# Optimization experiments

Measured on AMD Instinct MI355X. Metric: run time of the kernel, lower is better.

## Reference

```python
import jax, jax.numpy as jnp
import numpy as np

EPS = 1e-8  # torch.cosine_similarity eps


def setup_inputs() -> dict:
    key = jax.random.key(0)
    kq, km, ki = jax.random.split(key, 3)
    B, N, D = 512, 131072, 512
    query = jax.random.normal(kq, (B, D), dtype=jnp.float32)
    memory_matrix = jax.random.normal(km, (N, D), dtype=jnp.float32)
    importance = jax.random.uniform(ki, (N,), dtype=jnp.float32)
    return {"query": query, "memory_matrix": memory_matrix, "importance": importance, "k": 16}


def reference(query, memory_matrix, importance, k):
    # Cosine similarity (torch semantics: dot / max(|q||m|, eps))
    q_norm = jnp.linalg.norm(query, axis=-1)            # [B]
    m_norm = jnp.linalg.norm(memory_matrix, axis=-1)    # [N]
    dots = jnp.einsum('bd,nd->bn', query, memory_matrix)  # [B, N]
    sims = dots / jnp.maximum(q_norm[:, None] * m_norm[None, :], EPS)
    # Importance boosting
    boosted = sims * (1.0 + 0.3 * importance)[None, :]
    # Top-k retrieval + gather of memory contents
    vals, idx = jax.lax.top_k(boosted, k)               # [B, k]
    gathered = memory_matrix[idx]                        # [B, k, D]
    return vals, gathered
```

## Files before the change

kernel.cpp:

```cpp
#include <hip/hip_runtime.h>
#include <hip/hip_bf16.h>
#include <math.h>

#define BQ 512
#define DIM 512
#define NMEM 131072
#define TOPK 16

#define BM 128
#define BN 128
#define BK 32
#define KSTEPS (DIM / BK)
#define NSUB 8
#define CHUNK_N (BN * NSUB)
#define CHUNKS (NMEM / CHUNK_N)
#define BTILES (BQ / BM)
#define CAP 32
#define CAPF 24
#define RESCORE 32
#define LDSTR 40
#define NEG_INF (-3.402823466e38f)

typedef unsigned short u16;
typedef unsigned int u32;
typedef short bf16x8 __attribute__((ext_vector_type(8)));
typedef float f32x4 __attribute__((ext_vector_type(4)));

static __device__ inline u32 pack2(float a, float b) {
  __hip_bfloat162 p = __float22bfloat162_rn(make_float2(a, b));
  return *(u32*)&p;
}

static __device__ inline void gl_lds16(const void* g, void* l) {
  __builtin_amdgcn_global_load_lds(
      (const __attribute__((address_space(1))) u32*)g,
      (__attribute__((address_space(3))) u32*)l, 16, 0, 0);
}

__global__ __launch_bounds__(256) void prep_kernel(const float* __restrict__ q,
                                                   float* __restrict__ inv_qn,
                                                   u16* __restrict__ qb) {
  int row = blockIdx.x * 4 + (threadIdx.x >> 6);
  int lane = threadIdx.x & 63;
  const float4* r4 = (const float4*)(q + (size_t)row * DIM);
  float4 x0 = r4[lane * 2], x1 = r4[lane * 2 + 1];
  float ss = x0.x * x0.x + x0.y * x0.y + x0.z * x0.z + x0.w * x0.w +
             x1.x * x1.x + x1.y * x1.y + x1.z * x1.z + x1.w * x1.w;
#pragma unroll
  for (int off = 32; off; off >>= 1) ss += __shfl_down(ss, off);
  if (lane == 0) inv_qn[row] = 1.0f / sqrtf(ss);
  uint4 w;
  w.x = pack2(x0.x, x0.y);
  w.y = pack2(x0.z, x0.w);
  w.z = pack2(x1.x, x1.y);
  w.w = pack2(x1.z, x1.w);
  *(uint4*)(qb + (size_t)row * DIM + lane * 8) = w;
}

__global__ __launch_bounds__(256) void convert_kernel(
    const float* __restrict__ mem, const float* __restrict__ imp,
    u16* __restrict__ membf, float* __restrict__ colscale) {
  int row = blockIdx.x * 4 + (threadIdx.x >> 6);
  int lane = threadIdx.x & 63;
  const float4* r4 = (const float4*)(mem + (size_t)row * DIM);
  float4 x0 = r4[lane * 2], x1 = r4[lane * 2 + 1];
  float ss = x0.x * x0.x + x0.y * x0.y + x0.z * x0.z + x0.w * x0.w +
             x1.x * x1.x + x1.y * x1.y + x1.z * x1.z + x1.w * x1.w;
  uint4 w;
  w.x = pack2(x0.x, x0.y);
  w.y = pack2(x0.z, x0.w);
  w.z = pack2(x1.x, x1.y);
  w.w = pack2(x1.z, x1.w);
  *(uint4*)(membf + (size_t)row * DIM + lane * 8) = w;
#pragma unroll
  for (int off = 32; off; off >>= 1) ss += __shfl_down(ss, off);
  if (lane == 0) colscale[row] = (1.0f + 0.3f * imp[row]) / sqrtf(ss);
}

static __device__ inline void mfma_step(const u16* Asb, const u16* Bsb, int wm,
                                        int wn, int c16, int quad,
                                        f32x4 acc[4][4]) {
  bf16x8 af[4], bfr[4];
  const int ksw = (quad ^ (c16 & 3)) * 8;
#pragma unroll
  for (int mi = 0; mi < 4; ++mi)
    af[mi] = *(const bf16x8*)&Asb[(wm * 64 + mi * 16 + c16) * BK + ksw];
#pragma unroll
  for (int ni = 0; ni < 4; ++ni)
    bfr[ni] = *(const bf16x8*)&Bsb[(wn * 64 + ni * 16 + c16) * BK + ksw];
#pragma unroll
  for (int mi = 0; mi < 4; ++mi)
#pragma unroll
    for (int ni = 0; ni < 4; ++ni)
      acc[mi][ni] = __builtin_amdgcn_mfma_f32_16x16x32_bf16(af[mi], bfr[ni],
                                                            acc[mi][ni], 0, 0, 0);
}

static __device__ inline void stage4(const u16* ag0, const u16* ag1,
                                     const u16* bg0, const u16* bg1, u16* Asb,
                                     u16* Bsb, int blk0, int blk1, int koff) {
  gl_lds16(ag0 + koff, Asb + blk0 * 512);
  gl_lds16(ag1 + koff, Asb + blk1 * 512);
  gl_lds16(bg0 + koff, Bsb + blk0 * 512);
  gl_lds16(bg1 + koff, Bsb + blk1 * 512);
}

__global__ __launch_bounds__(256, 2) void main_fast(
    const u16* __restrict__ qb, const u16* __restrict__ membf,
    const float* __restrict__ cs, const float* __restrict__ inv_qn,
    float* __restrict__ part_v, int* __restrict__ part_i) {
  __shared__ __align__(16) u16 As[2][BM * BK];
  __shared__ __align__(16) u16 Bs[2][BN * BK];
  __shared__ float topv[BM][TOPK];
  __shared__ int topi[BM][TOPK];
  __shared__ float cbv[BM * CAPF];
  __shared__ int cbi[BM * CAPF];
  __shared__ float cutoff[BM];
  __shared__ int cnt[BM];
  __shared__ float qn_s[BM];
  __shared__ int again;

  const int tid = threadIdx.x;
  const int lane = tid & 63, wid = tid >> 6;
  const int wm = wid >> 1, wn = wid & 1;
  const int c16 = lane & 15, quad = lane >> 4;

  const int lin = blockIdx.x;
  const int btile = (lin >> 3) & 3;
  const int chunk = (lin & 7) + ((lin >> 5) << 3);
  const int bbase = btile * BM;

  for (int e = tid; e < BM * TOPK; e += 256) {
    topv[e >> 4][e & 15] = NEG_INF;
    topi[e >> 4][e & 15] = -1;
  }
  if (tid < BM) {
    cutoff[tid] = NEG_INF;
    cnt[tid] = 0;
    qn_s[tid] = inv_qn[bbase + tid];
  }
  if (tid == 0) again = 0;
  __syncthreads();

  float qnl[16];
#pragma unroll
  for (int ii = 0; ii < 16; ++ii)
    qnl[ii] = qn_s[wm * 64 + (ii >> 2) * 16 + quad * 4 + (ii & 3)];

  const int blk0 = wid * 2, blk1 = wid * 2 + 1;
  const int rin = lane >> 2;
  const int sr0 = blk0 * 16 + rin;
  const int sr1 = blk1 * 16 + rin;
  const int skof = (((lane & 3) ^ (rin & 3)) * 8);
  const u16* ag0 = qb + (size_t)(bbase + sr0) * DIM + skof;
  const u16* ag1 = qb + (size_t)(bbase + sr1) * DIM + skof;

  for (int sub = 0; sub < NSUB; ++sub) {
    const int n0g = chunk * CHUNK_N + sub * BN;
    const u16* bg0 = membf + (size_t)(n0g + sr0) * DIM + skof;
    const u16* bg1 = membf + (size_t)(n0g + sr1) * DIM + skof;

    f32x4 acc[4][4];
#pragma unroll
    for (int mi = 0; mi < 4; ++mi)
#pragma unroll
      for (int ni = 0; ni < 4; ++ni) acc[mi][ni] = (f32x4){0.f, 0.f, 0.f, 0.f};

    stage4(ag0, ag1, bg0, bg1, &As[0][0], &Bs[0][0], blk0, blk1, 0);
    __syncthreads();

    for (int kp = 0; kp < KSTEPS / 2; ++kp) {
      stage4(ag0, ag1, bg0, bg1, &As[1][0], &Bs[1][0], blk0, blk1,
             (2 * kp + 1) * BK);
      mfma_step(&As[0][0], &Bs[0][0], wm, wn, c16, quad, acc);
      __syncthreads();
      if (kp + 1 < KSTEPS / 2)
        stage4(ag0, ag1, bg0, bg1, &As[0][0], &Bs[0][0], blk0, blk1,
               (2 * kp + 2) * BK);
      mfma_step(&As[1][0], &Bs[1][0], wm, wn, c16, quad, acc);
      __syncthreads();
    }

    float scl[4];
    int gcol[4];
#pragma unroll
    for (int ni = 0; ni < 4; ++ni) {
      const int c = n0g + wn * 64 + ni * 16 + c16;
      scl[ni] = cs[c];
      gcol[ni] = c;
    }
#pragma unroll
    for (int mi = 0; mi < 4; ++mi)
#pragma unroll
      for (int ni = 0; ni < 4; ++ni)
#pragma unroll
        for (int reg = 0; reg < 4; ++reg)
          acc[mi][ni][reg] *= qnl[mi * 4 + reg] * scl[ni];

    unsigned long long consumed = 0ull;
    for (;;) {
      float cutl[16];
#pragma unroll
      for (int ii = 0; ii < 16; ++ii)
        cutl[ii] = cutoff[wm * 64 + (ii >> 2) * 16 + quad * 4 + (ii & 3)];
#pragma unroll
      for (int mi = 0; mi < 4; ++mi)
#pragma unroll
        for (int reg = 0; reg < 4; ++reg) {
          const int r = wm * 64 + mi * 16 + quad * 4 + reg;
          const float cl = cutl[mi * 4 + reg];
#pragma unroll
          for (int ni = 0; ni < 4; ++ni) {
            const int bit = mi * 16 + ni * 4 + reg;
            const float v = acc[mi][ni][reg];
            if (!((consumed >> bit) & 1ull) && v > cl) {
              int pos = atomicAdd(&cnt[r], 1);
              if (pos < CAPF) {
                cbv[r * CAPF + pos] = v;
                cbi[r * CAPF + pos] = gcol[ni];
                consumed |= 1ull << bit;
              }
            }
          }
        }
      __syncthreads();
      if (tid < BM) {
        const int r = tid;
        const int m = cnt[r];
        const int take = m < CAPF ? m : CAPF;
        for (int c = 0; c < take; ++c) {
          const float v = cbv[r * CAPF + c];
          const int id = cbi[r * CAPF + c];
          if (v > topv[r][TOPK - 1]) {
            int j = TOPK - 1;
            while (j > 0 && topv[r][j - 1] < v) {
              topv[r][j] = topv[r][j - 1];
              topi[r][j] = topi[r][j - 1];
              --j;
            }
            topv[r][j] = v;
            topi[r][j] = id;
          }
        }
        cutoff[r] = topv[r][TOPK - 1];
        if (m > CAPF) again = 1;
        cnt[r] = 0;
      }
      __syncthreads();
      const int more = again;
      __syncthreads();
      if (tid == 0) again = 0;
      if (!more) break;
    }
  }

  for (int e = tid; e < BM * TOPK; e += 256) {
    const int r = e >> 4, j = e & 15;
    const size_t o = ((size_t)(bbase + r) * CHUNKS + chunk) * TOPK + j;
    part_v[o] = topv[r][j];
    part_i[o] = topi[r][j];
  }
}

__global__ __launch_bounds__(256, 2) void main_kernel(
    const u16* __restrict__ qb, const float* __restrict__ mem,
    const float* __restrict__ imp, const float* __restrict__ inv_qn,
    float* __restrict__ part_v, int* __restrict__ part_i) {
  __shared__ __align__(16) u16 As[BM * LDSTR];
  __shared__ __align__(16) u16 Bs[BN * LDSTR];
  __shared__ float topv[BM][TOPK];
  __shared__ int topi[BM][TOPK];
  __shared__ float cbv[BM * CAP];
  __shared__ int cbi[BM * CAP];
  __shared__ float cutoff[BM];
  __shared__ int cnt[BM];
  __shared__ float qn_s[BM];
  __shared__ float msum[BM * 4];
  __shared__ float colscale[BN];
  __shared__ int again;

  const int tid = threadIdx.x;
  const int lane = tid & 63, wid = tid >> 6;
  const int wm = wid >> 1, wn = wid & 1;
  const int c16 = lane & 15, quad = lane >> 4;

  const int lin = blockIdx.x;
  const int btile = (lin >> 3) & 3;
  const int chunk = (lin & 7) + ((lin >> 5) << 3);
  const int bbase = btile * BM;

  for (int e = tid; e < BM * TOPK; e += 256) {
    topv[e >> 4][e & 15] = NEG_INF;
    topi[e >> 4][e & 15] = -1;
  }
  if (tid < BM) {
    cutoff[tid] = NEG_INF;
    cnt[tid] = 0;
    qn_s[tid] = inv_qn[bbase + tid];
  }
  if (tid == 0) again = 0;
  __syncthreads();

  float qnl[16];
#pragma unroll
  for (int ii = 0; ii < 16; ++ii)
    qnl[ii] = qn_s[wm * 64 + (ii >> 2) * 16 + quad * 4 + (ii & 3)];

  const int arow = tid >> 2, akc = tid & 3;
  const u16* qsrc0 = qb + (size_t)(bbase + arow) * DIM + akc * 8;
  const u16* qsrc1 = qsrc0 + (size_t)64 * DIM;
  u16* adst0 = As + arow * LDSTR + akc * 8;
  u16* adst1 = adst0 + 64 * LDSTR;
  u16* bdst0 = Bs + arow * LDSTR + akc * 8;
  u16* bdst1 = bdst0 + 64 * LDSTR;

  for (int sub = 0; sub < NSUB; ++sub) {
    const int n0g = chunk * CHUNK_N + sub * BN;
    const float* bsrc0 = mem + (size_t)(n0g + arow) * DIM + akc * 8;
    const float* bsrc1 = bsrc0 + (size_t)64 * DIM;

    f32x4 acc[4][4];
#pragma unroll
    for (int mi = 0; mi < 4; ++mi)
#pragma unroll
      for (int ni = 0; ni < 4; ++ni) acc[mi][ni] = (f32x4){0.f, 0.f, 0.f, 0.f};
    float ss0 = 0.f, ss1 = 0.f;

    for (int kt = 0; kt < DIM / BK; ++kt) {
      const int k0 = kt * BK;
      uint4 qa0 = *(const uint4*)(qsrc0 + k0);
      uint4 qa1 = *(const uint4*)(qsrc1 + k0);
      float4 b0a = *(const float4*)(bsrc0 + k0);
      float4 b0b = *(const float4*)(bsrc0 + k0 + 4);
      float4 b1a = *(const float4*)(bsrc1 + k0);
      float4 b1b = *(const float4*)(bsrc1 + k0 + 4);
      ss0 += b0a.x * b0a.x + b0a.y * b0a.y + b0a.z * b0a.z + b0a.w * b0a.w +
             b0b.x * b0b.x + b0b.y * b0b.y + b0b.z * b0b.z + b0b.w * b0b.w;
      ss1 += b1a.x * b1a.x + b1a.y * b1a.y + b1a.z * b1a.z + b1a.w * b1a.w +
             b1b.x * b1b.x + b1b.y * b1b.y + b1b.z * b1b.z + b1b.w * b1b.w;
      __syncthreads();
      *(uint4*)adst0 = qa0;
      *(uint4*)adst1 = qa1;
      uint4 w0, w1;
      w0.x = pack2(b0a.x, b0a.y); w0.y = pack2(b0a.z, b0a.w);
      w0.z = pack2(b0b.x, b0b.y); w0.w = pack2(b0b.z, b0b.w);
      w1.x = pack2(b1a.x, b1a.y); w1.y = pack2(b1a.z, b1a.w);
      w1.z = pack2(b1b.x, b1b.y); w1.w = pack2(b1b.z, b1b.w);
      *(uint4*)bdst0 = w0;
      *(uint4*)bdst1 = w1;
      __syncthreads();
      bf16x8 af[4], bfr[4];
#pragma unroll
      for (int mi = 0; mi < 4; ++mi)
        af[mi] = *(const bf16x8*)&As[(wm * 64 + mi * 16 + c16) * LDSTR + quad * 8];
#pragma unroll
      for (int ni = 0; ni < 4; ++ni)
        bfr[ni] = *(const bf16x8*)&Bs[(wn * 64 + ni * 16 + c16) * LDSTR + quad * 8];
#pragma unroll
      for (int mi = 0; mi < 4; ++mi)
#pragma unroll
        for (int ni = 0; ni < 4; ++ni)
          acc[mi][ni] = __builtin_amdgcn_mfma_f32_16x16x32_bf16(
              af[mi], bfr[ni], acc[mi][ni], 0, 0, 0);
    }

    msum[arow * 4 + akc] = ss0;
    msum[(arow + 64) * 4 + akc] = ss1;
    __syncthreads();
    if (tid < BN)
      colscale[tid] = (1.0f + 0.3f * imp[n0g + tid]) /
                      sqrtf(msum[tid * 4] + msum[tid * 4 + 1] +
                            msum[tid * 4 + 2] + msum[tid * 4 + 3]);
    __syncthreads();

    float scl[4];
    int gcol[4];
#pragma unroll
    for (int ni = 0; ni < 4; ++ni) {
      scl[ni] = colscale[wn * 64 + ni * 16 + c16];
      gcol[ni] = n0g + wn * 64 + ni * 16 + c16;
    }
#pragma unroll
    for (int mi = 0; mi < 4; ++mi)
#pragma unroll
      for (int ni = 0; ni < 4; ++ni)
#pragma unroll
        for (int reg = 0; reg < 4; ++reg)
          acc[mi][ni][reg] *= qnl[mi * 4 + reg] * scl[ni];

    unsigned long long consumed = 0ull;
    for (;;) {
      float cutl[16];
#pragma unroll
      for (int ii = 0; ii < 16; ++ii)
        cutl[ii] = cutoff[wm * 64 + (ii >> 2) * 16 + quad * 4 + (ii & 3)];
#pragma unroll
      for (int mi = 0; mi < 4; ++mi)
#pragma unroll
        for (int reg = 0; reg < 4; ++reg) {
          const int r = wm * 64 + mi * 16 + quad * 4 + reg;
          const float cl = cutl[mi * 4 + reg];
#pragma unroll
          for (int ni = 0; ni < 4; ++ni) {
            const int bit = mi * 16 + ni * 4 + reg;
            const float v = acc[mi][ni][reg];
            if (!((consumed >> bit) & 1ull) && v > cl) {
              int pos = atomicAdd(&cnt[r], 1);
              if (pos < CAP) {
                cbv[r * CAP + pos] = v;
                cbi[r * CAP + pos] = gcol[ni];
                consumed |= 1ull << bit;
              }
            }
          }
        }
      __syncthreads();
      if (tid < BM) {
        const int r = tid;
        const int m = cnt[r];
        const int take = m < CAP ? m : CAP;
        for (int c = 0; c < take; ++c) {
          const float v = cbv[r * CAP + c];
          const int id = cbi[r * CAP + c];
          if (v > topv[r][TOPK - 1]) {
            int j = TOPK - 1;
            while (j > 0 && topv[r][j - 1] < v) {
              topv[r][j] = topv[r][j - 1];
              topi[r][j] = topi[r][j - 1];
              --j;
            }
            topv[r][j] = v;
            topi[r][j] = id;
          }
        }
        cutoff[r] = topv[r][TOPK - 1];
        if (m > CAP) again = 1;
        cnt[r] = 0;
      }
      __syncthreads();
      const int more = again;
      __syncthreads();
      if (tid == 0) again = 0;
      if (!more) break;
    }
  }

  for (int e = tid; e < BM * TOPK; e += 256) {
    const int r = e >> 4, j = e & 15;
    const size_t o = ((size_t)(bbase + r) * CHUNKS + chunk) * TOPK + j;
    part_v[o] = topv[r][j];
    part_i[o] = topi[r][j];
  }
}

#define CAND (CHUNKS * TOPK)
__global__ __launch_bounds__(256) void final_kernel(
    const float* __restrict__ part_v, const int* __restrict__ part_i,
    const float* __restrict__ mem, const float* __restrict__ query,
    const float* __restrict__ imp, const float* __restrict__ inv_qn,
    float* __restrict__ out) {
  __shared__ float cv[CAND];
  __shared__ int ci[CAND];
  __shared__ float q_s[DIM];
  __shared__ float rv[4];
  __shared__ int rp[4];
  __shared__ float exv[RESCORE];
  __shared__ int exi[RESCORE];
  __shared__ float selv[TOPK];
  __shared__ int seli[TOPK];
  const int b = blockIdx.x, tid = threadIdx.x;
  const int lane = tid & 63, wid = tid >> 6;
  const size_t base = (size_t)b * CAND;
  for (int e = tid; e < CAND; e += 256) {
    cv[e] = part_v[base + e];
    ci[e] = part_i[base + e];
  }
  q_s[tid] = query[(size_t)b * DIM + tid];
  q_s[tid + 256] = query[(size_t)b * DIM + 256 + tid];
  __syncthreads();

  for (int j = 0; j < RESCORE; ++j) {
    float best = NEG_INF;
    int bp = 0;
    for (int e = tid; e < CAND; e += 256)
      if (cv[e] > best) { best = cv[e]; bp = e; }
#pragma unroll
    for (int off = 32; off; off >>= 1) {
      float ov = __shfl_down(best, off);
      int op = __shfl_down(bp, off);
      if (ov > best) { best = ov; bp = op; }
    }
    if (lane == 0) { rv[wid] = best; rp[wid] = bp; }
    __syncthreads();
    if (tid == 0) {
      float bb = rv[0];
      int pp = rp[0];
      for (int w = 1; w < 4; ++w)
        if (rv[w] > bb) { bb = rv[w]; pp = rp[w]; }
      exi[j] = ci[pp];
      cv[pp] = NEG_INF;
    }
    __syncthreads();
  }

  const float iq = inv_qn[b];
  for (int jj = wid; jj < RESCORE; jj += 4) {
    const int idx = exi[jj];
    const float4* mr = (const float4*)(mem + (size_t)idx * DIM);
    float4 m0 = mr[lane * 2], m1 = mr[lane * 2 + 1];
    float4 q0 = *(const float4*)&q_s[lane * 8];
    float4 q1 = *(const float4*)&q_s[lane * 8 + 4];
    float dt = m0.x * q0.x + m0.y * q0.y + m0.z * q0.z + m0.w * q0.w +
               m1.x * q1.x + m1.y * q1.y + m1.z * q1.z + m1.w * q1.w;
    float mm = m0.x * m0.x + m0.y * m0.y + m0.z * m0.z + m0.w * m0.w +
               m1.x * m1.x + m1.y * m1.y + m1.z * m1.z + m1.w * m1.w;
#pragma unroll
    for (int off = 32; off; off >>= 1) {
      dt += __shfl_down(dt, off);
      mm += __shfl_down(mm, off);
    }
    if (lane == 0)
      exv[jj] = dt * iq * (1.0f + 0.3f * imp[idx]) / sqrtf(mm);
  }
  __syncthreads();

  if (tid == 0) {
    u32 used = 0;
    for (int j = 0; j < TOPK; ++j) {
      float bb = NEG_INF;
      int pp = -1;
      for (int c = 0; c < RESCORE; ++c) {
        if ((used >> c) & 1u) continue;
        const float v = exv[c];
        if (v > bb || (pp >= 0 && v == bb && exi[c] < exi[pp])) { bb = v; pp = c; }
      }
      used |= 1u << pp;
      selv[j] = bb;
      seli[j] = exi[pp];
    }
  }
  __syncthreads();
  if (tid < TOPK) out[(size_t)b * TOPK + tid] = selv[tid];
  for (int e = tid; e < TOPK * (DIM / 4); e += 256) {
    const int j = e >> 7, t = e & 127;
    const float4* src = (const float4*)(mem + (size_t)seli[j] * DIM);
    float4* dst = (float4*)(out + (size_t)BQ * TOPK + ((size_t)b * TOPK + j) * DIM);
    dst[t] = src[t];
  }
}

extern "C" void kernel_launch(void* const* d_in, const int* in_sizes, int n_in,
                              void* d_out, int out_size, void* d_ws, size_t ws_size,
                              hipStream_t stream) {
  const float* query = (const float*)d_in[0];
  const float* mem = (const float*)d_in[1];
  const float* imp = (const float*)d_in[2];
  float* out = (float*)d_out;

  char* ws = (char*)d_ws;
  float* inv_qn = (float*)ws;
  u16* qb = (u16*)(ws + 2048);
  float* part_v = (float*)(ws + 2048 + (size_t)BQ * DIM * 2);
  int* part_i = (int*)((char*)part_v + (size_t)BQ * CHUNKS * TOPK * 4);
  char* extra = (char*)part_i + (size_t)BQ * CHUNKS * TOPK * 4;
  const size_t used = (size_t)(extra - ws);
  const size_t fast_need =
      used + (size_t)NMEM * 4 + (size_t)NMEM * DIM * 2;

  hipLaunchKernelGGL(prep_kernel, dim3(BQ / 4), dim3(256), 0, stream,
                     query, inv_qn, qb);
  if (ws_size >= fast_need) {
    float* colscale = (float*)extra;
    u16* membf = (u16*)(extra + (size_t)NMEM * 4);
    hipLaunchKernelGGL(convert_kernel, dim3(NMEM / 4), dim3(256), 0, stream,
                       mem, imp, membf, colscale);
    hipLaunchKernelGGL(main_fast, dim3(BTILES * CHUNKS), dim3(256), 0, stream,
                       qb, membf, colscale, inv_qn, part_v, part_i);
  } else {
    hipLaunchKernelGGL(main_kernel, dim3(BTILES * CHUNKS), dim3(256), 0, stream,
                       qb, mem, imp, inv_qn, part_v, part_i);
  }
  hipLaunchKernelGGL(final_kernel, dim3(BQ), dim3(256), 0, stream,
                     part_v, part_i, mem, query, imp, inv_qn, out);
}
```

Baseline: 826.3 us.

## Prefetch GEMM tiles two steps ahead across sub-tiles with vmcnt-based waits

```diff
diff --git a/kernel.cpp b/kernel.cpp
--- a/kernel.cpp
+++ b/kernel.cpp
@@ -78,31 +78,20 @@
 }
 
 static __device__ inline void mfma_step(const u16* Asb, const u16* Bsb, int wm,
-                                        int wn, int c16, int quad,
-                                        f32x4 acc[4][4]) {
+                                        int wn, int lane, f32x4 acc[4][4]) {
   bf16x8 af[4], bfr[4];
-  const int ksw = (quad ^ (c16 & 3)) * 8;
 #pragma unroll
   for (int mi = 0; mi < 4; ++mi)
-    af[mi] = *(const bf16x8*)&Asb[(wm * 64 + mi * 16 + c16) * BK + ksw];
+    af[mi] = *(const bf16x8*)&Asb[((wm << 2) + mi) * 512 + (lane << 3)];
 #pragma unroll
   for (int ni = 0; ni < 4; ++ni)
-    bfr[ni] = *(const bf16x8*)&Bsb[(wn * 64 + ni * 16 + c16) * BK + ksw];
+    bfr[ni] = *(const bf16x8*)&Bsb[((wn << 2) + ni) * 512 + (lane << 3)];
 #pragma unroll
   for (int mi = 0; mi < 4; ++mi)
 #pragma unroll
     for (int ni = 0; ni < 4; ++ni)
       acc[mi][ni] = __builtin_amdgcn_mfma_f32_16x16x32_bf16(af[mi], bfr[ni],
                                                             acc[mi][ni], 0, 0, 0);
-}
-
-static __device__ inline void stage4(const u16* ag0, const u16* ag1,
-                                     const u16* bg0, const u16* bg1, u16* Asb,
-                                     u16* Bsb, int blk0, int blk1, int koff) {
-  gl_lds16(ag0 + koff, Asb + blk0 * 512);
-  gl_lds16(ag1 + koff, Asb + blk1 * 512);
-  gl_lds16(bg0 + koff, Bsb + blk0 * 512);
-  gl_lds16(bg1 + koff, Bsb + blk1 * 512);
 }
 
 __global__ __launch_bounds__(256, 2) void main_fast(
@@ -130,6 +119,28 @@
   const int chunk = (lin & 7) + ((lin >> 5) << 3);
   const int bbase = btile * BM;
 
+  const int blk0 = wid * 2;
+  const u16* agA0 = qb + (size_t)(bbase + blk0 * 16 + (lane & 15)) * DIM +
+                    (lane >> 4) * 8;
+  const u16* bgB0 = membf +
+                    (size_t)(chunk * CHUNK_N + blk0 * 16 + (lane & 15)) * DIM +
+                    (lane >> 4) * 8;
+
+  auto STAGE = [&](int gs) {
+    const int p = gs & 1;
+    const size_t ao = (size_t)(gs & 15) * BK;
+    const size_t bo = (size_t)(gs >> 4) * (BN * DIM) + ao;
+    u16* Ad = &As[p][0] + blk0 * 512;
+    u16* Bd = &Bs[p][0] + blk0 * 512;
+    gl_lds16(agA0 + ao, Ad);
+    gl_lds16(agA0 + ao + (size_t)16 * DIM, Ad + 512);
+    gl_lds16(bgB0 + bo, Bd);
+    gl_lds16(bgB0 + bo + (size_t)16 * DIM, Bd + 512);
+  };
+
+  STAGE(0);
+  STAGE(1);
+
   for (int e = tid; e < BM * TOPK; e += 256) {
     topv[e >> 4][e & 15] = NEG_INF;
     topi[e >> 4][e & 15] = -1;
@@ -147,18 +158,8 @@
   for (int ii = 0; ii < 16; ++ii)
     qnl[ii] = qn_s[wm * 64 + (ii >> 2) * 16 + quad * 4 + (ii & 3)];
 
-  const int blk0 = wid * 2, blk1 = wid * 2 + 1;
-  const int rin = lane >> 2;
-  const int sr0 = blk0 * 16 + rin;
-  const int sr1 = blk1 * 16 + rin;
-  const int skof = (((lane & 3) ^ (rin & 3)) * 8);
-  const u16* ag0 = qb + (size_t)(bbase + sr0) * DIM + skof;
-  const u16* ag1 = qb + (size_t)(bbase + sr1) * DIM + skof;
-
   for (int sub = 0; sub < NSUB; ++sub) {
     const int n0g = chunk * CHUNK_N + sub * BN;
-    const u16* bg0 = membf + (size_t)(n0g + sr0) * DIM + skof;
-    const u16* bg1 = membf + (size_t)(n0g + sr1) * DIM + skof;
 
     f32x4 acc[4][4];
 #pragma unroll
@@ -166,19 +167,22 @@
 #pragma unroll
       for (int ni = 0; ni < 4; ++ni) acc[mi][ni] = (f32x4){0.f, 0.f, 0.f, 0.f};
 
-    stage4(ag0, ag1, bg0, bg1, &As[0][0], &Bs[0][0], blk0, blk1, 0);
-    __syncthreads();
-
-    for (int kp = 0; kp < KSTEPS / 2; ++kp) {
-      stage4(ag0, ag1, bg0, bg1, &As[1][0], &Bs[1][0], blk0, blk1,
-             (2 * kp + 1) * BK);
-      mfma_step(&As[0][0], &Bs[0][0], wm, wn, c16, quad, acc);
-      __syncthreads();
-      if (kp + 1 < KSTEPS / 2)
-        stage4(ag0, ag1, bg0, bg1, &As[0][0], &Bs[0][0], blk0, blk1,
-               (2 * kp + 2) * BK);
-      mfma_step(&As[1][0], &Bs[1][0], wm, wn, c16, quad, acc);
-      __syncthreads();
+    for (int th = 0; th < KSTEPS / 2; ++th) {
+      const int gs0 = sub * KSTEPS + th * 2;
+      const int gs1 = gs0 + 1;
+      asm volatile("s_waitcnt vmcnt(4)" ::: "memory");
+      __builtin_amdgcn_s_barrier();
+      mfma_step(&As[0][0], &Bs[0][0], wm, wn, lane, acc);
+      __builtin_amdgcn_s_barrier();
+      if (gs0 + 2 <= NSUB * KSTEPS - 1) STAGE(gs0 + 2);
+      if (gs1 == NSUB * KSTEPS - 1)
+        asm volatile("s_waitcnt vmcnt(0)" ::: "memory");
+      else
+        asm volatile("s_waitcnt vmcnt(4)" ::: "memory");
+      __builtin_amdgcn_s_barrier();
+      mfma_step(&As[1][0], &Bs[1][0], wm, wn, lane, acc);
+      __builtin_amdgcn_s_barrier();
+      if (gs1 + 2 <= NSUB * KSTEPS - 1) STAGE(gs1 + 2);
     }
 
     float scl[4];
```

Result: slower. 853.1 us (+3.2%).
